# Optimization experiments

Hardware: AMD Instinct MI355X
Metric: run time of the kernel (lower is better)

Reference implementation:

```python
import jax, jax.numpy as jnp
import numpy as np
from jax import lax

E4M3 = jnp.float8_e4m3fn
DIM_NUMS = (((1,), (0,)), ((), ()))  # contract inputs last dim with kernel first dim


def quantize_dequantize(x, q_dtype, scale, compute_dtype):
    dtype_max = jnp.finfo(q_dtype).max.astype(compute_dtype)
    s = scale.astype(compute_dtype)
    scaled = x.astype(compute_dtype) / s
    clipped = jnp.clip(scaled, -dtype_max, dtype_max)
    qx = clipped.astype(q_dtype)
    # dequantize back to x.dtype
    return qx.astype(x.dtype) * scale.astype(x.dtype)


def setup_inputs() -> dict:
    key = jax.random.key(0)
    k1, k2 = jax.random.split(key)
    H = 1024  # amax_history_length
    return {
        "inputs": jax.random.normal(k1, (8192, 4096), dtype=jnp.float32),
        "kernel": jax.random.normal(k2, (4096, 4096), dtype=jnp.float32),
        "input_scale": jnp.ones((1,), jnp.float32),
        "input_amax_history": jnp.zeros((H,), jnp.float32),
        "kernel_scale": jnp.ones((1,), jnp.float32),
        "kernel_amax_history": jnp.zeros((H,), jnp.float32),
        "output_grad_scale": jnp.ones((1,), jnp.float32),
        "output_grad_amax_history": jnp.zeros((H,), jnp.float32),
    }


def reference(inputs, kernel, input_scale, input_amax_history, kernel_scale,
              kernel_amax_history, output_grad_scale, output_grad_amax_history):
    comp_dtype = kernel.dtype
    inputs = jnp.asarray(inputs, comp_dtype)
    # in_qdq on both operands (e4m3); out_qdq is identity in the forward pass.
    lhs_qdq = quantize_dequantize(inputs, E4M3, input_scale, comp_dtype)
    rhs_qdq = quantize_dequantize(kernel, E4M3, kernel_scale, comp_dtype)
    out = lax.dot_general(lhs_qdq, rhs_qdq, DIM_NUMS, precision=None)
    return out
```

## Files before the change

kernel.cpp:

```cpp
#include <hip/hip_runtime.h>
#include <stdint.h>

#define M_DIM 8192
#define N_DIM 4096
#define K_DIM 4096
#define NT (K_DIM / 128)

typedef float f32x4 __attribute__((ext_vector_type(4)));
typedef int v4i __attribute__((ext_vector_type(4)));
typedef int v8i __attribute__((ext_vector_type(8)));
typedef uint32_t u32;


__device__ __forceinline__ void gload_lds16(const void* g, void* l) {
  __builtin_amdgcn_global_load_lds(
      (__attribute__((address_space(1))) void*)(g),
      (__attribute__((address_space(3))) void*)(l), 16, 0, 0);
}

__device__ __forceinline__ float clipdiv(float v, float s) {
  v = v / s;
  return fminf(fmaxf(v, -448.f), 448.f);
}

__device__ __forceinline__ u32 pack4_fp8(float a, float b, float c, float d) {
  int w = __builtin_amdgcn_cvt_pk_fp8_f32(a, b, 0, false);
  w = __builtin_amdgcn_cvt_pk_fp8_f32(c, d, w, true);
  return (u32)w;
}

__device__ __forceinline__ v8i rd8(const void* lo, const void* hi) {
  v4i l = *(const v4i*)lo;
  v4i h = *(const v4i*)hi;
  return __builtin_shufflevector(l, h, 0, 1, 2, 3, 4, 5, 6, 7);
}

__device__ __forceinline__ f32x4 mfma8(v8i a, v8i b, f32x4 c) {
  return __builtin_amdgcn_mfma_scale_f32_16x16x128_f8f6f4(
      a, b, c, 0, 0, 0, 0x7f7f7f7f, 0, 0x7f7f7f7f);
}


__global__ __launch_bounds__(256) void quant_a(const float* __restrict__ x,
                                               u32* __restrict__ q,
                                               const float* __restrict__ scale,
                                               int nv4) {
  int base = blockIdx.x * 1024 + threadIdx.x;
  float s = scale[0];
#pragma unroll
  for (int r = 0; r < 4; ++r) {
    int idx = base + r * 256;
    if (idx < nv4) {
      float4 v = ((const float4*)x)[idx];
      q[idx] = pack4_fp8(clipdiv(v.x, s), clipdiv(v.y, s),
                         clipdiv(v.z, s), clipdiv(v.w, s));
    }
  }
}


__global__ __launch_bounds__(256) void quant_b_t(const float* __restrict__ B,
                                                 uint8_t* __restrict__ qT,
                                                 const float* __restrict__ scale) {
  __shared__ u32 lt[64 * 17];
  int tid = threadIdx.x;
  int kt = blockIdx.x * 64;
  int nt = blockIdx.y * 64;
  float s = scale[0];

  int kq = tid >> 4;
  int nq = tid & 15;
  int k0 = kq * 4, n0 = nq * 4;
  const float* src = B + (long)(kt + k0) * N_DIM + nt + n0;
  float4 v0 = *(const float4*)(src);
  float4 v1 = *(const float4*)(src + N_DIM);
  float4 v2 = *(const float4*)(src + 2 * N_DIM);
  float4 v3 = *(const float4*)(src + 3 * N_DIM);

  lt[(n0 + 0) * 17 + kq] = pack4_fp8(clipdiv(v0.x, s), clipdiv(v1.x, s),
                                     clipdiv(v2.x, s), clipdiv(v3.x, s));
  lt[(n0 + 1) * 17 + kq] = pack4_fp8(clipdiv(v0.y, s), clipdiv(v1.y, s),
                                     clipdiv(v2.y, s), clipdiv(v3.y, s));
  lt[(n0 + 2) * 17 + kq] = pack4_fp8(clipdiv(v0.z, s), clipdiv(v1.z, s),
                                     clipdiv(v2.z, s), clipdiv(v3.z, s));
  lt[(n0 + 3) * 17 + kq] = pack4_fp8(clipdiv(v0.w, s), clipdiv(v1.w, s),
                                     clipdiv(v2.w, s), clipdiv(v3.w, s));
  __syncthreads();

  int n = tid >> 2, ch = tid & 3;
  uint4 o;
  o.x = lt[n * 17 + ch * 4 + 0];
  o.y = lt[n * 17 + ch * 4 + 1];
  o.z = lt[n * 17 + ch * 4 + 2];
  o.w = lt[n * 17 + ch * 4 + 3];
  *(uint4*)&qT[(long)(nt + n) * K_DIM + kt + ch * 16] = o;
}


template <int BUF>
__device__ __forceinline__ void stage_tile(const uint8_t* const (&gA)[4],
                                           const uint8_t* const (&gB)[4],
                                           uint8_t* lds, const int (&ldo)[4],
                                           long ko) {
#pragma unroll
  for (int r = 0; r < 4; ++r)
    gload_lds16(gA[r] + ko, lds + BUF * 32768 + ldo[r]);
#pragma unroll
  for (int r = 0; r < 4; ++r)
    gload_lds16(gB[r] + ko, lds + 65536 + BUF * 32768 + ldo[r]);
}

template <int BUF>
__device__ __forceinline__ void compute_tile(const uint8_t* lds,
                                             const int (&offA)[8][2],
                                             const int (&offB)[4][2],
                                             f32x4 (&acc)[8][4]) {
  const uint8_t* Ab = lds + BUF * 32768;
  const uint8_t* Bb = lds + 65536 + BUF * 32768;
  v8i b[4];
#pragma unroll
  for (int j = 0; j < 4; ++j) b[j] = rd8(Bb + offB[j][0], Bb + offB[j][1]);
#pragma unroll
  for (int h = 0; h < 2; ++h) {
    v8i a[4];
#pragma unroll
    for (int i = 0; i < 4; ++i)
      a[i] = rd8(Ab + offA[h * 4 + i][0], Ab + offA[h * 4 + i][1]);
#pragma unroll
    for (int i = 0; i < 4; ++i)
#pragma unroll
      for (int j = 0; j < 4; ++j)
        acc[h * 4 + i][j] = mfma8(a[i], b[j], acc[h * 4 + i][j]);
  }
}

__global__ __launch_bounds__(512, 2) void gemm_mx(const uint8_t* __restrict__ Aq,
                                                  const uint8_t* __restrict__ BqT,
                                                  float* __restrict__ C,
                                                  const float* __restrict__ sA,
                                                  const float* __restrict__ sB) {
  __shared__ __align__(16) uint8_t lds[131072];

  const int tid = threadIdx.x;
  const int lane = tid & 63;
  const int wid = tid >> 6;
  const int wr = wid >> 2;
  const int wc = wid & 3;
  const int r16 = lane & 15;
  const int hi = lane >> 4;

  int bid = blockIdx.x;
  int wg = (bid & 7) * 64 + (bid >> 3);
  const long bm = (long)(wg >> 4) * 256;
  const long bn = (long)(wg & 15) * 256;

  float s = sA[0] * sB[0];
  asm volatile("" ::"v"(s));

  const uint8_t* gA[4];
  const uint8_t* gB[4];
  int ldo[4];
#pragma unroll
  for (int r = 0; r < 4; ++r) {
    int gid = tid + 512 * r;
    int row = gid >> 3, gc = gid & 7;
    int sc = (gc ^ (row & 7)) << 4;
    gA[r] = Aq + (bm + row) * (long)K_DIM + sc;
    gB[r] = BqT + (bn + row) * (long)K_DIM + sc;
    ldo[r] = gid * 16;
  }

  int offA[8][2], offB[4][2];
#pragma unroll
  for (int mi = 0; mi < 8; ++mi) {
    int ra = wr * 128 + mi * 16 + r16;
#pragma unroll
    for (int g = 0; g < 2; ++g) {
      int lg = 2 * hi + g;
      offA[mi][g] = ra * 128 + ((lg ^ (ra & 7)) << 4);
    }
  }
#pragma unroll
  for (int nj = 0; nj < 4; ++nj) {
    int rb = wc * 64 + nj * 16 + r16;
#pragma unroll
    for (int g = 0; g < 2; ++g) {
      int lg = 2 * hi + g;
      offB[nj][g] = rb * 128 + ((lg ^ (rb & 7)) << 4);
    }
  }

  f32x4 acc[8][4] = {};

  stage_tile<0>(gA, gB, lds, ldo, 0);
  asm volatile("s_waitcnt vmcnt(0)" ::: "memory");
  __builtin_amdgcn_s_barrier();

  for (int i = 0; i < NT / 2; ++i) {
    long ko1 = (long)((2 * i + 1) & (NT - 1)) * 128;
    stage_tile<1>(gA, gB, lds, ldo, ko1);
    compute_tile<0>(lds, offA, offB, acc);
    asm volatile("s_waitcnt vmcnt(0)" ::: "memory");
    __builtin_amdgcn_s_barrier();

    long ko2 = (long)((2 * i + 2) & (NT - 1)) * 128;
    stage_tile<0>(gA, gB, lds, ldo, ko2);
    compute_tile<1>(lds, offA, offB, acc);
    asm volatile("s_waitcnt vmcnt(0)" ::: "memory");
    __builtin_amdgcn_s_barrier();
  }

  const float sc = s;
#pragma unroll
  for (int mi = 0; mi < 8; ++mi)
#pragma unroll
    for (int nj = 0; nj < 4; ++nj) {
      long row = bm + wr * 128 + mi * 16 + hi * 4;
      long col = bn + wc * 64 + nj * 16 + r16;
      float* cp = C + row * N_DIM + col;
      f32x4 v = acc[mi][nj];
#pragma unroll
      for (int q = 0; q < 4; ++q) cp[(long)q * N_DIM] = v[q] * sc;
    }
}


extern "C" void kernel_launch(void* const* d_in, const int* in_sizes, int n_in,
                              void* d_out, int out_size, void* d_ws, size_t ws_size,
                              hipStream_t stream) {
  const float* A = (const float*)d_in[0];
  const float* B = (const float*)d_in[1];
  const float* sA = (const float*)d_in[2];
  const float* sB = (const float*)d_in[4];
  float* out = (float*)d_out;

  uint8_t* Aq = (uint8_t*)d_ws;
  uint8_t* BqT = Aq + (size_t)M_DIM * K_DIM;

  int nv4_a = M_DIM * K_DIM / 4;
  quant_a<<<nv4_a / 1024, 256, 0, stream>>>(A, (u32*)Aq, sA, nv4_a);
  quant_b_t<<<dim3(K_DIM / 64, N_DIM / 64), 256, 0, stream>>>(B, BqT, sB);
  gemm_mx<<<dim3((M_DIM / 256) * (N_DIM / 256)), 512, 0, stream>>>(Aq, BqT, out, sA, sB);
}
```

Measured before the change: 188.9 us.

## Load B fragments directly from global into registers, halve LDS footprint

The GEMM no longer stages the B tile through LDS. Each lane now reads its B fragment (32 bytes per row per k-tile) straight from global memory into registers, while A keeps the double-buffered LDS path, so LDS use drops from 128KB to 64KB. The aim is to cut LDS traffic and footprint, possibly allowing more resident workgroups. The cost is that B is no longer shared across waves: the 2 wave-rows now each fetch it from global/L2, and the global load latency is not prefetched ahead, since it is issued in the same iteration it is consumed and covered by the same vmcnt(0) wait.

```diff
diff --git a/kernel.cpp b/kernel.cpp
--- a/kernel.cpp
+++ b/kernel.cpp
@@ -98,28 +98,26 @@
 
 
 template <int BUF>
-__device__ __forceinline__ void stage_tile(const uint8_t* const (&gA)[4],
-                                           const uint8_t* const (&gB)[4],
-                                           uint8_t* lds, const int (&ldo)[4],
-                                           long ko) {
+__device__ __forceinline__ void stage_a(const uint8_t* const (&gA)[4],
+                                        uint8_t* lds, const int (&ldo)[4],
+                                        long ko) {
 #pragma unroll
   for (int r = 0; r < 4; ++r)
     gload_lds16(gA[r] + ko, lds + BUF * 32768 + ldo[r]);
-#pragma unroll
-  for (int r = 0; r < 4; ++r)
-    gload_lds16(gB[r] + ko, lds + 65536 + BUF * 32768 + ldo[r]);
+}
+
+__device__ __forceinline__ void load_b(v8i (&b)[4],
+                                       const uint8_t* const (&pB)[4], long ko) {
+#pragma unroll
+  for (int j = 0; j < 4; ++j) b[j] = rd8(pB[j] + ko, pB[j] + ko + 16);
 }
 
 template <int BUF>
 __device__ __forceinline__ void compute_tile(const uint8_t* lds,
                                              const int (&offA)[8][2],
-                                             const int (&offB)[4][2],
+                                             const v8i (&b)[4],
                                              f32x4 (&acc)[8][4]) {
   const uint8_t* Ab = lds + BUF * 32768;
-  const uint8_t* Bb = lds + 65536 + BUF * 32768;
-  v8i b[4];
-#pragma unroll
-  for (int j = 0; j < 4; ++j) b[j] = rd8(Bb + offB[j][0], Bb + offB[j][1]);
 #pragma unroll
   for (int h = 0; h < 2; ++h) {
     v8i a[4];
@@ -139,7 +137,7 @@
                                                   float* __restrict__ C,
                                                   const float* __restrict__ sA,
                                                   const float* __restrict__ sB) {
-  __shared__ __align__(16) uint8_t lds[131072];
+  __shared__ __align__(16) uint8_t lds[65536];
 
   const int tid = threadIdx.x;
   const int lane = tid & 63;
@@ -158,7 +156,6 @@
   asm volatile("" ::"v"(s));
 
   const uint8_t* gA[4];
-  const uint8_t* gB[4];
   int ldo[4];
 #pragma unroll
   for (int r = 0; r < 4; ++r) {
@@ -166,11 +163,10 @@
     int row = gid >> 3, gc = gid & 7;
     int sc = (gc ^ (row & 7)) << 4;
     gA[r] = Aq + (bm + row) * (long)K_DIM + sc;
-    gB[r] = BqT + (bn + row) * (long)K_DIM + sc;
     ldo[r] = gid * 16;
   }
 
-  int offA[8][2], offB[4][2];
+  int offA[8][2];
 #pragma unroll
   for (int mi = 0; mi < 8; ++mi) {
     int ra = wr * 128 + mi * 16 + r16;
@@ -180,37 +176,43 @@
       offA[mi][g] = ra * 128 + ((lg ^ (ra & 7)) << 4);
     }
   }
+
+  const uint8_t* pB[4];
 #pragma unroll
   for (int nj = 0; nj < 4; ++nj) {
-    int rb = wc * 64 + nj * 16 + r16;
-#pragma unroll
-    for (int g = 0; g < 2; ++g) {
-      int lg = 2 * hi + g;
-      offB[nj][g] = rb * 128 + ((lg ^ (rb & 7)) << 4);
-    }
+    long rb = bn + wc * 64 + nj * 16 + r16;
+    pB[nj] = BqT + rb * (long)K_DIM + hi * 32;
   }
 
   f32x4 acc[8][4] = {};
 
-  stage_tile<0>(gA, gB, lds, ldo, 0);
+  stage_a<0>(gA, lds, ldo, 0);
   asm volatile("s_waitcnt vmcnt(0)" ::: "memory");
   __builtin_amdgcn_s_barrier();
 
   for (int i = 0; i < NT / 2; ++i) {
-    long ko1 = (long)((2 * i + 1) & (NT - 1)) * 128;
-    stage_tile<1>(gA, gB, lds, ldo, ko1);
-    compute_tile<0>(lds, offA, offB, acc);
-    asm volatile("s_waitcnt vmcnt(0)" ::: "memory");
-    __builtin_amdgcn_s_barrier();
-
-    long ko2 = (long)((2 * i + 2) & (NT - 1)) * 128;
-    stage_tile<0>(gA, gB, lds, ldo, ko2);
-    compute_tile<1>(lds, offA, offB, acc);
-    asm volatile("s_waitcnt vmcnt(0)" ::: "memory");
-    __builtin_amdgcn_s_barrier();
-  }
-
-  const float sc = s;
+    {
+      long kt0 = (long)(2 * i) * 128;
+      long kt1 = (long)((2 * i + 1) & (NT - 1)) * 128;
+      v8i b[4];
+      load_b(b, pB, kt0);
+      stage_a<1>(gA, lds, ldo, kt1);
+      compute_tile<0>(lds, offA, b, acc);
+      asm volatile("s_waitcnt vmcnt(0)" ::: "memory");
+      __builtin_amdgcn_s_barrier();
+    }
+    {
+      long kt1 = (long)(2 * i + 1) * 128;
+      long kt2 = (long)((2 * i + 2) & (NT - 1)) * 128;
+      v8i b[4];
+      load_b(b, pB, kt1);
+      stage_a<0>(gA, lds, ldo, kt2);
+      compute_tile<1>(lds, offA, b, acc);
+      asm volatile("s_waitcnt vmcnt(0)" ::: "memory");
+      __builtin_amdgcn_s_barrier();
+    }
+  }
+
 #pragma unroll
   for (int mi = 0; mi < 8; ++mi)
 #pragma unroll
@@ -220,7 +222,7 @@
       float* cp = C + row * N_DIM + col;
       f32x4 v = acc[mi][nj];
 #pragma unroll
-      for (int q = 0; q < 4; ++q) cp[(long)q * N_DIM] = v[q] * sc;
+      for (int q = 0; q < 4; ++q) cp[(long)q * N_DIM] = v[q] * s;
     }
 }
 
```

New measurement: 262.3 us. +38.8%, slower.
